# Kernel tuning notes

Hardware: AMD Instinct MI355X
Metric: run time of the kernel (lower is better)

## Reference

```python
import jax, jax.numpy as jnp
import numpy as np
import math

WS = 8          # window_size
H = 16          # num_heads
C = 512         # dim
D = C // H      # head dim


def _relative_coords_table():
    # (2*WS-1, 2*WS-1, 2), Swin-V2 log-spaced continuous coords
    r = jnp.arange(-(WS - 1), WS, dtype=jnp.float32)
    t = jnp.stack(jnp.meshgrid(r, r, indexing='ij'), axis=-1)
    t = t / (WS - 1) * 8.0
    return jnp.sign(t) * jnp.log2(jnp.abs(t) + 1.0) / np.float32(np.log2(8.0))


def _relative_position_index():
    # (WS*WS, WS*WS) int32 indices into the (2*WS-1)^2 bias table
    coords = np.stack(np.meshgrid(np.arange(WS), np.arange(WS), indexing='ij'))  # (2,WS,WS)
    cf = coords.reshape(2, -1)                                # (2, N)
    rel = cf[:, :, None] - cf[:, None, :]                     # (2, N, N)
    rel = rel.transpose(1, 2, 0)                              # (N, N, 2)
    rel[:, :, 0] += WS - 1
    rel[:, :, 1] += WS - 1
    rel[:, :, 0] *= 2 * WS - 1
    return jnp.asarray(rel.sum(-1), dtype=jnp.int32)


def setup_inputs() -> dict:
    key = jax.random.key(0)
    ks = jax.random.split(key, 9)
    B, N = 2048, WS * WS
    s = 0.02
    return {
        'hidden_states': jax.random.normal(ks[0], (B, N, C), jnp.float32),
        'q_w': jax.random.normal(ks[1], (C, C), jnp.float32) * s,
        'q_b': jnp.zeros((C,), jnp.float32),
        'k_w': jax.random.normal(ks[2], (C, C), jnp.float32) * s,
        'v_w': jax.random.normal(ks[3], (C, C), jnp.float32) * s,
        'v_b': jnp.zeros((C,), jnp.float32),
        'logit_scale': jnp.full((H, 1, 1), np.float32(math.log(10.0))),
        'cpb_w1': jax.random.normal(ks[4], (512, 2), jnp.float32) * s,
        'cpb_b1': jnp.zeros((512,), jnp.float32),
        'cpb_w2': jax.random.normal(ks[5], (H, 512), jnp.float32) * s,
    }


def reference(hidden_states, q_w, q_b, k_w, v_w, v_b, logit_scale,
              cpb_w1, cpb_b1, cpb_w2):
    B, N, _ = hidden_states.shape

    def heads(x):  # (B,N,C) -> (B,H,N,D)
        return x.reshape(B, N, H, D).transpose(0, 2, 1, 3)

    q = heads(hidden_states @ q_w.T + q_b)
    k = heads(hidden_states @ k_w.T)
    v = heads(hidden_states @ v_w.T + v_b)

    # cosine-similarity attention with clamped learnable logit scale
    qn = q / jnp.linalg.norm(q, axis=-1, keepdims=True)
    kn = k / jnp.linalg.norm(k, axis=-1, keepdims=True)
    scale = jnp.exp(jnp.minimum(logit_scale, np.float32(math.log(100.0))))  # (H,1,1)
    scores = jnp.einsum('bhnd,bhmd->bhnm', qn, kn) * scale

    # continuous relative position bias MLP + gather + sigmoid scale
    table = _relative_coords_table().reshape(-1, 2)            # (225, 2)
    hbias = jax.nn.relu(table @ cpb_w1.T + cpb_b1) @ cpb_w2.T  # (225, H)
    idx = _relative_position_index().reshape(-1)               # (N*N,)
    rpb = hbias[idx].reshape(N, N, H).transpose(2, 0, 1)       # (H, N, N)
    scores = scores + 16.0 * jax.nn.sigmoid(rpb)[None]

    probs = jax.nn.softmax(scores, axis=-1)
    ctx = jnp.einsum('bhnm,bhmd->bhnd', probs, v)
    return ctx.transpose(0, 2, 1, 3).reshape(B, N, C)
```

## Files before the change

kernel.cpp:

```cpp
#include <hip/hip_runtime.h>
#include <hip/hip_bf16.h>
#include <cstdint>
#include <cstddef>

typedef __attribute__((ext_vector_type(4))) float f32x4;
typedef __attribute__((ext_vector_type(8))) short short8;
typedef unsigned short ushort_t;

__device__ __forceinline__ ushort_t f2bf(float f) {
  unsigned u = __builtin_bit_cast(unsigned, f);
  u = u + 0x7FFFu + ((u >> 16) & 1u);
  return (ushort_t)(u >> 16);
}
__device__ __forceinline__ void load_lds16(const void* g, void* l) {
  __builtin_amdgcn_global_load_lds((const __attribute__((address_space(1))) void*)g,
                                   (__attribute__((address_space(3))) void*)l, 16, 0, 0);
}

__device__ __forceinline__ int swzA(int row, int b) { return row*128 + (b ^ ((row & 7) << 4)); }
__device__ __forceinline__ int swzQ(int row, int b) { return row*64  + (b ^ (((row >> 1) & 3) << 4)); }
__device__ __forceinline__ int swzV(int d,   int b) { return d*256   + (b ^ ((d & 7) << 4)); }

__global__ __launch_bounds__(256) void k_cvt_bf16(const float4* __restrict__ in,
                                                  ushort_t* __restrict__ outp, int n4) {
  int i = blockIdx.x * 256 + threadIdx.x;
  int stride = gridDim.x * 256;
  for (; i < n4; i += stride) {
    float4 v = in[i];
    ushort4 o = { f2bf(v.x), f2bf(v.y), f2bf(v.z), f2bf(v.w) };
    *(ushort4*)(outp + (size_t)i * 4) = o;
  }
}

__global__ __launch_bounds__(256) void k_wcat(const float* __restrict__ qw, const float* __restrict__ qb,
                                              const float* __restrict__ kw, const float* __restrict__ vw,
                                              const float* __restrict__ vb,
                                              ushort_t* __restrict__ Wcat, float* __restrict__ bcat) {
  int o = blockIdx.x;
  int h = o / 96, r = o % 96;
  const float* src; float bias;
  if (r < 32)      { src = qw + (size_t)(h*32 + r)      * 512; bias = qb[h*32 + r]; }
  else if (r < 64) { src = kw + (size_t)(h*32 + r - 32) * 512; bias = 0.f; }
  else             { src = vw + (size_t)(h*32 + r - 64) * 512; bias = vb[h*32 + r - 64]; }
  int t = threadIdx.x;
  Wcat[(size_t)o*512 + t]       = f2bf(src[t]);
  Wcat[(size_t)o*512 + t + 256] = f2bf(src[t + 256]);
  if (t == 0) bcat[o] = bias;
}

__global__ __launch_bounds__(256) void k_bias(const float* __restrict__ w1, const float* __restrict__ b1,
                                              const float* __restrict__ w2, float* __restrict__ bias16) {
  int t = blockIdx.x;
  int a = t / 15, b = t % 15;
  float x = (float)(a - 7) * (8.f / 7.f);
  float y = (float)(b - 7) * (8.f / 7.f);
  float fx = (x == 0.f) ? 0.f : copysignf(log2f(fabsf(x) + 1.f) * (1.f / 3.f), x);
  float fy = (y == 0.f) ? 0.f : copysignf(log2f(fabsf(y) + 1.f) * (1.f / 3.f), y);
  int wv = threadIdx.x >> 6, lane = threadIdx.x & 63;
  float acc[4] = {0.f, 0.f, 0.f, 0.f};
  for (int it = 0; it < 8; ++it) {
    int j = it*64 + lane;
    float act = fmaxf(fx * w1[2*j] + fy * w1[2*j + 1] + b1[j], 0.f);
#pragma unroll
    for (int hh = 0; hh < 4; ++hh)
      acc[hh] += act * w2[(wv*4 + hh)*512 + j];
  }
#pragma unroll
  for (int hh = 0; hh < 4; ++hh) {
    float v = acc[hh];
    for (int s = 1; s < 64; s <<= 1) v += __shfl_xor(v, s);
    if (lane == 0) bias16[t*16 + wv*4 + hh] = 16.f / (1.f + __expf(-v));
  }
}

#define BS_OFF 16384
#define KS_OFF 8192
#define VT_OFF 16384
#define PS_OFF 24576

__global__ __launch_bounds__(256) void k_main(const ushort_t* __restrict__ hbf,
                                              const ushort_t* __restrict__ Wcat,
                                              const float* __restrict__ bcat,
                                              const float* __restrict__ bias16,
                                              const float* __restrict__ lscale,
                                              float* __restrict__ out) {
  __shared__ __align__(128) char lb_raw[32768];
  char* lb = lb_raw;

  int bid = blockIdx.x;
  int wg = (bid & 7) * 2048 + (bid >> 3);
  int mtile = wg >> 4;
  int h     = wg & 15;

  int tid = threadIdx.x;
  int w = tid >> 6, lane = tid & 63;
  int lm = lane & 15, lg = lane >> 4;

  const ushort_t* Ag = hbf  + (size_t)mtile * 128 * 512;
  const ushort_t* Wg = Wcat + (size_t)h * 96 * 512;

  int offA[4];
#pragma unroll
  for (int i = 0; i < 4; ++i) {
    int row = i*32 + (tid >> 3);
    int sl  = (tid & 7) ^ (row & 7);
    offA[i] = row*512 + sl*8;
  }

  f32x4 acc[2][6] = {};

  for (int ks = 0; ks < 8; ++ks) {
    int k0 = ks * 64;
#pragma unroll
    for (int i = 0; i < 4; ++i)
      load_lds16(Ag + offA[i] + k0, lb + i*4096 + w*1024);
#pragma unroll
    for (int i = 0; i < 3; ++i)
      load_lds16(Wg + offA[i] + k0, lb + BS_OFF + i*4096 + w*1024);
    __syncthreads();
#pragma unroll
    for (int ch = 0; ch < 2; ++ch) {
      int bo = ch*64 + lg*16;
      short8 av[2], bv[6];
#pragma unroll
      for (int i = 0; i < 2; ++i) av[i] = *(const short8*)(lb + swzA(w*32 + i*16 + lm, bo));
#pragma unroll
      for (int j = 0; j < 6; ++j) bv[j] = *(const short8*)(lb + BS_OFF + swzA(j*16 + lm, bo));
#pragma unroll
      for (int i = 0; i < 2; ++i)
#pragma unroll
        for (int j = 0; j < 6; ++j)
          acc[i][j] = __builtin_amdgcn_mfma_f32_16x16x32_bf16(av[i], bv[j], acc[i][j], 0, 0, 0);
    }
    __syncthreads();
  }

  __builtin_amdgcn_s_setprio(1);
  float scl = __expf(fminf(lscale[h], 4.6051701860f));
  float bb[6];
#pragma unroll
  for (int nj = 0; nj < 6; ++nj) bb[nj] = bcat[h*96 + nj*16 + lm];

#pragma unroll
  for (int i = 0; i < 2; ++i) {
#pragma unroll
    for (int r = 0; r < 4; ++r) {
      float q0 = acc[i][0][r] + bb[0], q1 = acc[i][1][r] + bb[1];
      float k0 = acc[i][2][r],         k1 = acc[i][3][r];
      float ssq = q0*q0 + q1*q1;
      float ssk = k0*k0 + k1*k1;
      ssq += __shfl_xor(ssq, 1); ssq += __shfl_xor(ssq, 2);
      ssq += __shfl_xor(ssq, 4); ssq += __shfl_xor(ssq, 8);
      ssk += __shfl_xor(ssk, 1); ssk += __shfl_xor(ssk, 2);
      ssk += __shfl_xor(ssk, 4); ssk += __shfl_xor(ssk, 8);
      float rq = rsqrtf(ssq) * scl;
      float rk = rsqrtf(ssk);
      int row = w*32 + i*16 + lg*4 + r;
      *(ushort_t*)(lb + swzQ(row, lm*2))                  = f2bf(q0 * rq);
      *(ushort_t*)(lb + swzQ(row, 32 + lm*2))             = f2bf(q1 * rq);
      *(ushort_t*)(lb + KS_OFF + swzQ(row, lm*2))         = f2bf(k0 * rk);
      *(ushort_t*)(lb + KS_OFF + swzQ(row, 32 + lm*2))    = f2bf(k1 * rk);
    }
#pragma unroll
    for (int j = 0; j < 2; ++j) {
      ushort4 pk;
      pk.x = f2bf(acc[i][4+j][0] + bb[4+j]);
      pk.y = f2bf(acc[i][4+j][1] + bb[4+j]);
      pk.z = f2bf(acc[i][4+j][2] + bb[4+j]);
      pk.w = f2bf(acc[i][4+j][3] + bb[4+j]);
      int d = j*16 + lm, tokb = (w*32 + i*16 + lg*4) * 2;
      *(ushort4*)(lb + VT_OFF + swzV(d, tokb)) = pk;
    }
  }
  __syncthreads();

  float bfrag[4][4];
#pragma unroll
  for (int ci = 0; ci < 4; ++ci) {
    int m = ci*16 + lm, rm = m >> 3, cm = m & 7;
#pragma unroll
    for (int r = 0; r < 4; ++r) {
      int n = w*16 + lg*4 + r;
      int idx = ((n >> 3) - rm + 7)*15 + ((n & 7) - cm + 7);
      bfrag[ci][r] = bias16[idx*16 + h];
    }
  }

#pragma unroll
  for (int win = 0; win < 2; ++win) {
    short8 aq = *(const short8*)(lb + swzQ(win*64 + w*16 + lm, lg*16));
    f32x4 p[4];
#pragma unroll
    for (int ci = 0; ci < 4; ++ci) {
      short8 bk = *(const short8*)(lb + KS_OFF + swzQ(win*64 + ci*16 + lm, lg*16));
      f32x4 z = {0.f, 0.f, 0.f, 0.f};
      f32x4 s = __builtin_amdgcn_mfma_f32_16x16x32_bf16(aq, bk, z, 0, 0, 0);
#pragma unroll
      for (int r = 0; r < 4; ++r)
        p[ci][r] = __expf(s[r] + bfrag[ci][r]);
    }
#pragma unroll
    for (int ci = 0; ci < 4; ++ci)
#pragma unroll
      for (int r = 0; r < 4; ++r) {
        int row = w*16 + lg*4 + r;
        *(ushort_t*)(lb + PS_OFF + swzA(row, (ci*16 + lm)*2)) = f2bf(p[ci][r]);
      }
    float rs[4];
#pragma unroll
    for (int r = 0; r < 4; ++r) {
      float s = p[0][r] + p[1][r] + p[2][r] + p[3][r];
      s += __shfl_xor(s, 1); s += __shfl_xor(s, 2);
      s += __shfl_xor(s, 4); s += __shfl_xor(s, 8);
      rs[r] = 1.f / s;
    }
    f32x4 oacc[2] = {};
#pragma unroll
    for (int kk = 0; kk < 2; ++kk) {
      short8 ap = *(const short8*)(lb + PS_OFF + swzA(w*16 + lm, kk*64 + lg*16));
#pragma unroll
      for (int ci = 0; ci < 2; ++ci) {
        short8 bvv = *(const short8*)(lb + VT_OFF + swzV(ci*16 + lm, win*128 + kk*64 + lg*16));
        oacc[ci] = __builtin_amdgcn_mfma_f32_16x16x32_bf16(ap, bvv, oacc[ci], 0, 0, 0);
      }
    }
    size_t gw = (size_t)mtile*2 + win;
#pragma unroll
    for (int ci = 0; ci < 2; ++ci)
#pragma unroll
      for (int r = 0; r < 4; ++r) {
        int n = w*16 + lg*4 + r;
        out[(gw*64 + n)*512 + h*32 + ci*16 + lm] = oacc[ci][r] * rs[r];
      }
  }
  __builtin_amdgcn_s_setprio(0);
}

extern "C" void kernel_launch(void* const* d_in, const int* in_sizes, int n_in,
                              void* d_out, int out_size, void* d_ws, size_t ws_size,
                              hipStream_t stream) {
  (void)in_sizes; (void)n_in; (void)out_size; (void)ws_size;
  const float* hidden = (const float*)d_in[0];
  const float* q_w    = (const float*)d_in[1];
  const float* q_b    = (const float*)d_in[2];
  const float* k_w    = (const float*)d_in[3];
  const float* v_w    = (const float*)d_in[4];
  const float* v_b    = (const float*)d_in[5];
  const float* lscale = (const float*)d_in[6];
  const float* cpb_w1 = (const float*)d_in[7];
  const float* cpb_b1 = (const float*)d_in[8];
  const float* cpb_w2 = (const float*)d_in[9];
  float* out = (float*)d_out;

  char* wsb = (char*)d_ws;
  ushort_t* hbf    = (ushort_t*)wsb;
  ushort_t* Wcat   = (ushort_t*)(wsb + 134217728);
  float*    bcat   = (float*)(wsb + 135790592);
  float*    bias16 = (float*)(wsb + 135796736);

  hipLaunchKernelGGL(k_cvt_bf16, dim3(2048), dim3(256), 0, stream,
                     (const float4*)hidden, hbf, 16777216);
  hipLaunchKernelGGL(k_wcat, dim3(1536), dim3(256), 0, stream,
                     q_w, q_b, k_w, v_w, v_b, Wcat, bcat);
  hipLaunchKernelGGL(k_bias, dim3(225), dim3(256), 0, stream,
                     cpb_w1, cpb_b1, cpb_w2, bias16);
  hipLaunchKernelGGL(k_main, dim3(16384), dim3(256), 0, stream,
                     hbf, Wcat, bcat, bias16, lscale, out);
}
```

Before: 485.7 us.

## Double-buffer QKV GEMM K-loop with 32-wide stages and async LDS prefetch

Replaces the single-buffered 64-wide K-step loop in the fused QKV projection with a 16-step loop over 32-wide K slices. Each slice is double-buffered in LDS, and the next stage's global→LDS loads are issued before waiting on the current one via explicit vmcnt waits and raw barriers. The goal is to overlap global load latency with the MFMA work instead of stalling on a full __syncthreads each iteration. In exchange there are twice as many barriers, a new swizzle for 64-byte rows, and hand-tuned waitcnt counts that depend on per-wave load counts (waves 0-1 issue an extra B load).

Result: faster. 472.3 us (-2.8%).

```diff
diff --git a/kernel.cpp b/kernel.cpp
--- a/kernel.cpp
+++ b/kernel.cpp
@@ -99,41 +99,58 @@
   const ushort_t* Ag = hbf  + (size_t)mtile * 128 * 512;
   const ushort_t* Wg = Wcat + (size_t)h * 96 * 512;
 
-  int offA[4];
-#pragma unroll
-  for (int i = 0; i < 4; ++i) {
-    int row = i*32 + (tid >> 3);
-    int sl  = (tid & 7) ^ (row & 7);
-    offA[i] = row*512 + sl*8;
-  }
+  int rA0 = w*32      + (lane >> 2);
+  int rA1 = w*32 + 16 + (lane >> 2);
+  int rB0 = w*16      + (lane >> 2);
+  int rB1 = 64 + w*16 + (lane >> 2);
+  int sl  = lane & 3;
+  int offA0 = rA0*512 + (sl ^ ((rA0 >> 1) & 3))*8;
+  int offA1 = rA1*512 + (sl ^ ((rA1 >> 1) & 3))*8;
+  int offB0 = rB0*512 + (sl ^ ((rB0 >> 1) & 3))*8;
+  int offB1 = rB1*512 + (sl ^ ((rB1 >> 1) & 3))*8;
 
   f32x4 acc[2][6] = {};
 
-  for (int ks = 0; ks < 8; ++ks) {
-    int k0 = ks * 64;
-#pragma unroll
-    for (int i = 0; i < 4; ++i)
-      load_lds16(Ag + offA[i] + k0, lb + i*4096 + w*1024);
-#pragma unroll
-    for (int i = 0; i < 3; ++i)
-      load_lds16(Wg + offA[i] + k0, lb + BS_OFF + i*4096 + w*1024);
-    __syncthreads();
-#pragma unroll
-    for (int ch = 0; ch < 2; ++ch) {
-      int bo = ch*64 + lg*16;
-      short8 av[2], bv[6];
-#pragma unroll
-      for (int i = 0; i < 2; ++i) av[i] = *(const short8*)(lb + swzA(w*32 + i*16 + lm, bo));
-#pragma unroll
-      for (int j = 0; j < 6; ++j) bv[j] = *(const short8*)(lb + BS_OFF + swzA(j*16 + lm, bo));
-#pragma unroll
-      for (int i = 0; i < 2; ++i)
-#pragma unroll
-        for (int j = 0; j < 6; ++j)
-          acc[i][j] = __builtin_amdgcn_mfma_f32_16x16x32_bf16(av[i], bv[j], acc[i][j], 0, 0, 0);
-    }
-    __syncthreads();
-  }
+#define STAGE(ksn, bsel) do {                                                  \
+    int kk0 = (ksn) * 32;                                                      \
+    load_lds16(Ag + offA0 + kk0, lb + (bsel)*8192 + (w*2+0)*1024);             \
+    load_lds16(Ag + offA1 + kk0, lb + (bsel)*8192 + (w*2+1)*1024);             \
+    load_lds16(Wg + offB0 + kk0, lb + BS_OFF + (bsel)*6144 + w*1024);          \
+    if (w < 2)                                                                 \
+      load_lds16(Wg + offB1 + kk0, lb + BS_OFF + (bsel)*6144 + (4+w)*1024);    \
+  } while (0)
+
+  STAGE(0, 0);
+#pragma unroll
+  for (int ks = 0; ks < 16; ++ks) {
+    int cur = ks & 1;
+    if (ks < 15) {
+      STAGE(ks + 1, cur ^ 1);
+      if (w < 2) asm volatile("s_waitcnt vmcnt(4)" ::: "memory");
+      else       asm volatile("s_waitcnt vmcnt(3)" ::: "memory");
+    } else {
+      asm volatile("s_waitcnt vmcnt(0)" ::: "memory");
+    }
+    asm volatile("s_barrier" ::: "memory");
+
+    const char* Ab = lb + cur*8192;
+    const char* Bb = lb + BS_OFF + cur*6144;
+    short8 av0 = *(const short8*)(Ab + swzQ(w*32      + lm, lg*16));
+    short8 av1 = *(const short8*)(Ab + swzQ(w*32 + 16 + lm, lg*16));
+    short8 bv[6];
+#pragma unroll
+    for (int j = 0; j < 6; ++j)
+      bv[j] = *(const short8*)(Bb + swzQ(j*16 + lm, lg*16));
+#pragma unroll
+    for (int j = 0; j < 6; ++j)
+      acc[0][j] = __builtin_amdgcn_mfma_f32_16x16x32_bf16(av0, bv[j], acc[0][j], 0, 0, 0);
+#pragma unroll
+    for (int j = 0; j < 6; ++j)
+      acc[1][j] = __builtin_amdgcn_mfma_f32_16x16x32_bf16(av1, bv[j], acc[1][j], 0, 0, 0);
+
+    asm volatile("s_barrier" ::: "memory");
+  }
+#undef STAGE
 
   __builtin_amdgcn_s_setprio(1);
   float scl = __expf(fminf(lscale[h], 4.6051701860f));
```
